# Optimization experiments

Measured on AMD Instinct MI355X. Metric: run time of the kernel, lower is better.

The kernel has to match this reference:

```python
import jax, jax.numpy as jnp
from jax import lax
import numpy as np

B, C, H, W = 16, 64, 256, 256
K = 4


def setup_inputs() -> dict:
    key = jax.random.key(0)
    k1, k2, k3, k4 = jax.random.split(key, 4)
    x = jax.random.normal(k1, (B, C, H, W), dtype=jnp.float32)
    weight = jax.random.normal(k2, (K, C, 3, 3), dtype=jnp.float32)
    # attn 1x1 conv: weight [K, C] (squeezed 1x1 spatial), bias [K]
    attn_w = jax.random.normal(k3, (K, C), dtype=jnp.float32) * (1.0 / np.sqrt(C))
    attn_b = jax.random.normal(k4, (K,), dtype=jnp.float32) * 0.01
    return {"x": x, "weight": weight, "attn_w": attn_w, "attn_b": attn_b}


def reference(x, weight, attn_w, attn_b):
    # 1x1 conv -> logits [B, K, H, W], then softmax over the K kernels
    logits = jnp.einsum("bchw,kc->bkhw", x, attn_w) + attn_b[None, :, None, None]
    attn = jax.nn.softmax(logits, axis=1)
    # One grouped call producing all K single-channel conv outputs: [B, K, H, W]
    conv = lax.conv_general_dilated(
        x, weight,
        window_strides=(1, 1), padding="SAME",
        dimension_numbers=("NCHW", "OIHW", "NCHW"),
    )
    # attention-weighted mixture, summed over kernels -> [B, 1, H, W]
    return jnp.sum(conv * attn, axis=1, keepdims=True)
```

## Files before the change

kernel.cpp:

```cpp
#include <hip/hip_runtime.h>


typedef _Float16 half2_t __attribute__((ext_vector_type(2)));
typedef unsigned int uint;

#define HH 256
#define WW 256
#define CH 64
#define PLANE (HH * WW)
#define NT 512
#define TR 32
#define TC 64
#define NG 32
#define ROWS 34
#define NC4 18
#define LDSS 73
#define BUF_DW (ROWS * LDSS)
#define TU (ROWS * NC4)
#define NS 2

#define WPK_N 1152
#define APK_OFF 1152

__device__ __forceinline__ uint pkrtz(float a, float b) {
    return __builtin_bit_cast(uint, __builtin_amdgcn_cvt_pkrtz(a, b));
}

__device__ __forceinline__ float dot2(uint a, uint b, float c) {
#if __has_builtin(__builtin_amdgcn_fdot2)
    return __builtin_amdgcn_fdot2(__builtin_bit_cast(half2_t, a),
                                  __builtin_bit_cast(half2_t, b), c, false);
#else
    half2_t ha = __builtin_bit_cast(half2_t, a);
    half2_t hb = __builtin_bit_cast(half2_t, b);
    return c + (float)ha[0] * (float)hb[0] + (float)ha[1] * (float)hb[1];
#endif
}

__global__ void kwdc_pack(const float* __restrict__ weight,
                          const float* __restrict__ attn_w,
                          uint* __restrict__ wsu) {
    int e = blockIdx.x * 256 + threadIdx.x;
    if (e < WPK_N) {
        int k = e / 288, rem = e % 288, pair = rem / 9, tap = rem % 9;
        int c0 = 2 * pair;
        wsu[e] = pkrtz(weight[(k * CH + c0) * 9 + tap],
                       weight[(k * CH + c0 + 1) * 9 + tap]);
    } else if (e < WPK_N + 128) {
        int e2 = e - WPK_N;
        int k = e2 / 32, pair = e2 % 32;
        int c0 = 2 * pair;
        wsu[APK_OFF + e2] = pkrtz(attn_w[k * CH + c0], attn_w[k * CH + c0 + 1]);
    }
}

__global__ __launch_bounds__(NT, 4) void kwdc_main(
    const float* __restrict__ x,
    const uint*  __restrict__ wsu,
    const float* __restrict__ attn_b,
    float* __restrict__ out)
{
    __shared__ uint lds[2][BUF_DW];

    const int tid = threadIdx.x;

    const int fid = blockIdx.x;
    const int tw = (fid >> 3) & 3;
    const int th = fid & 7;
    const int b  = fid >> 5;

    const int r  = tid >> 4;
    const int cg = tid & 15;
    const int wb = cg * 4;

    const int h0 = th * TR;
    const int w0 = tw * TC;

    const float* xb = x + (size_t)b * CH * PLANE;

    int  s_gofs[NS];
    int  s_lofs[NS];
    bool s_val[NS];
    bool s_act[NS];
#pragma unroll
    for (int s = 0; s < NS; ++s) {
        int i = tid + s * NT;
        bool act = i < TU;
        int col4 = i % NC4;
        int row  = i / NC4;
        int gh  = h0 + row - 1;
        int gw0 = w0 - 4 + col4 * 4;
        s_act[s]  = act;
        s_val[s]  = act && ((unsigned)gh < HH) && ((unsigned)gw0 < WW);
        s_gofs[s] = gh * WW + gw0;
        s_lofs[s] = row * LDSS + col4 * 4;
    }

    struct Unit { float4 a, b; };
    Unit stgA[NS], stgB[NS];

    auto load_set = [&](int g, Unit* stg) {
#pragma unroll
        for (int s = 0; s < NS; ++s) {
            float4 va = {0.f, 0.f, 0.f, 0.f}, vb = va;
            if (s_val[s]) {
                const float* pa = xb + (size_t)(2 * g) * PLANE + s_gofs[s];
                va = *reinterpret_cast<const float4*>(pa);
                vb = *reinterpret_cast<const float4*>(pa + PLANE);
            }
            stg[s].a = va; stg[s].b = vb;
        }
    };

    auto store_set = [&](const Unit* stg, int buf) {
#pragma unroll
        for (int s = 0; s < NS; ++s) {
            if (s_act[s]) {
                uint* q = &lds[buf][s_lofs[s]];
                q[0] = pkrtz(stg[s].a.x, stg[s].b.x);
                q[1] = pkrtz(stg[s].a.y, stg[s].b.y);
                q[2] = pkrtz(stg[s].a.z, stg[s].b.z);
                q[3] = pkrtz(stg[s].a.w, stg[s].b.w);
            }
        }
    };

    float conv[4][4];
    float logit[4][4];
#pragma unroll
    for (int k = 0; k < 4; ++k)
#pragma unroll
        for (int p = 0; p < 4; ++p) { conv[k][p] = 0.f; logit[k][p] = 0.f; }

    load_set(0, stgA);
    store_set(stgA, 0);
    load_set(1, stgA);
    load_set(2, stgB);
    __syncthreads();

    for (int g = 0; g < NG; ++g) {
        const uint* tp = &lds[g & 1][r * LDSS + wb + 3];
        uint rv[3][6];
#pragma unroll
        for (int i = 0; i < 3; ++i)
#pragma unroll
            for (int j = 0; j < 6; ++j)
                rv[i][j] = tp[i * LDSS + j];

        uint w2[4][9];
        uint a2[4];
#pragma unroll
        for (int k = 0; k < 4; ++k) {
            const uint* wq = wsu + k * 288 + g * 9;
#pragma unroll
            for (int t = 0; t < 9; ++t) w2[k][t] = wq[t];
            a2[k] = wsu[APK_OFF + k * 32 + g];
        }

        if (g + 1 < NG) {
            Unit* setp = (g & 1) ? stgB : stgA;
            store_set(setp, (g + 1) & 1);
            if (g + 3 < NG) load_set(g + 3, setp);
        }

#pragma unroll
        for (int k = 0; k < 4; ++k) {
#pragma unroll
            for (int p = 0; p < 4; ++p) {
                float acc = conv[k][p];
                acc = dot2(rv[0][p],     w2[k][0], acc);
                acc = dot2(rv[0][p + 1], w2[k][1], acc);
                acc = dot2(rv[0][p + 2], w2[k][2], acc);
                acc = dot2(rv[1][p],     w2[k][3], acc);
                acc = dot2(rv[1][p + 1], w2[k][4], acc);
                acc = dot2(rv[1][p + 2], w2[k][5], acc);
                acc = dot2(rv[2][p],     w2[k][6], acc);
                acc = dot2(rv[2][p + 1], w2[k][7], acc);
                acc = dot2(rv[2][p + 2], w2[k][8], acc);
                conv[k][p] = acc;
                logit[k][p] = dot2(rv[1][p + 1], a2[k], logit[k][p]);
            }
        }
        __syncthreads();
    }

    const float b0 = attn_b[0], b1 = attn_b[1], b2 = attn_b[2], b3 = attn_b[3];
    float4 o;
    float* op = &o.x;
#pragma unroll
    for (int p = 0; p < 4; ++p) {
        float l0 = logit[0][p] + b0;
        float l1 = logit[1][p] + b1;
        float l2 = logit[2][p] + b2;
        float l3 = logit[3][p] + b3;
        float m = fmaxf(fmaxf(l0, l1), fmaxf(l2, l3));
        float e0 = __expf(l0 - m), e1 = __expf(l1 - m);
        float e2 = __expf(l2 - m), e3 = __expf(l3 - m);
        float s = e0 + e1 + e2 + e3;
        float num = conv[0][p] * e0 + conv[1][p] * e1
                  + conv[2][p] * e2 + conv[3][p] * e3;
        op[p] = num / s;
    }
    size_t oidx = (size_t)b * PLANE + (size_t)(h0 + r) * WW + (w0 + wb);
    *reinterpret_cast<float4*>(out + oidx) = o;
}

extern "C" void kernel_launch(void* const* d_in, const int* in_sizes, int n_in,
                              void* d_out, int out_size, void* d_ws, size_t ws_size,
                              hipStream_t stream) {
    const float* x      = (const float*)d_in[0];
    const float* weight = (const float*)d_in[1];
    const float* attn_w = (const float*)d_in[2];
    const float* attn_b = (const float*)d_in[3];
    float* out = (float*)d_out;
    uint*  wsu = (uint*)d_ws;

    kwdc_pack<<<dim3(5), 256, 0, stream>>>(weight, attn_w, wsu);
    kwdc_main<<<dim3(512), NT, 0, stream>>>(x, wsu, attn_b, out);
}
```

Baseline: 84.57 us.

## Retile to full-width 8-row strips to drop column halo loads

```diff
diff --git a/kernel.cpp b/kernel.cpp
--- a/kernel.cpp
+++ b/kernel.cpp
@@ -9,13 +9,12 @@
 #define CH 64
 #define PLANE (HH * WW)
 #define NT 512
-#define TR 32
-#define TC 64
+#define SR 8
+#define ROWS 10
 #define NG 32
-#define ROWS 34
-#define NC4 18
-#define LDSS 73
-#define BUF_DW (ROWS * LDSS)
+#define NC4 64
+#define P 259
+#define BUF_DW (ROWS * P)
 #define TU (ROWS * NC4)
 #define NS 2
 
@@ -65,16 +64,14 @@
     const int tid = threadIdx.x;
 
     const int fid = blockIdx.x;
-    const int tw = (fid >> 3) & 3;
-    const int th = fid & 7;
-    const int b  = fid >> 5;
-
-    const int r  = tid >> 4;
-    const int cg = tid & 15;
+    const int b   = fid & 15;
+    const int s   = fid >> 4;
+
+    const int h0 = s * SR;
+
+    const int tr = tid >> 6;
+    const int cg = tid & 63;
     const int wb = cg * 4;
-
-    const int h0 = th * TR;
-    const int w0 = tw * TC;
 
     const float* xb = x + (size_t)b * CH * PLANE;
 
@@ -83,17 +80,16 @@
     bool s_val[NS];
     bool s_act[NS];
 #pragma unroll
-    for (int s = 0; s < NS; ++s) {
-        int i = tid + s * NT;
+    for (int q = 0; q < NS; ++q) {
+        int i = tid + q * NT;
         bool act = i < TU;
-        int col4 = i % NC4;
-        int row  = i / NC4;
+        int col4 = i & 63;
+        int row  = i >> 6;
         int gh  = h0 + row - 1;
-        int gw0 = w0 - 4 + col4 * 4;
-        s_act[s]  = act;
-        s_val[s]  = act && ((unsigned)gh < HH) && ((unsigned)gw0 < WW);
-        s_gofs[s] = gh * WW + gw0;
-        s_lofs[s] = row * LDSS + col4 * 4;
+        s_act[q]  = act;
+        s_val[q]  = act && ((unsigned)gh < HH);
+        s_gofs[q] = gh * WW + col4 * 4;
+        s_lofs[q] = row * P + col4 * 4 + 1;
     }
 
     struct Unit { float4 a, b; };
@@ -101,26 +97,26 @@
 
     auto load_set = [&](int g, Unit* stg) {
 #pragma unroll
-        for (int s = 0; s < NS; ++s) {
+        for (int q = 0; q < NS; ++q) {
             float4 va = {0.f, 0.f, 0.f, 0.f}, vb = va;
-            if (s_val[s]) {
-                const float* pa = xb + (size_t)(2 * g) * PLANE + s_gofs[s];
+            if (s_val[q]) {
+                const float* pa = xb + (size_t)(2 * g) * PLANE + s_gofs[q];
                 va = *reinterpret_cast<const float4*>(pa);
                 vb = *reinterpret_cast<const float4*>(pa + PLANE);
             }
-            stg[s].a = va; stg[s].b = vb;
+            stg[q].a = va; stg[q].b = vb;
         }
     };
 
     auto store_set = [&](const Unit* stg, int buf) {
 #pragma unroll
-        for (int s = 0; s < NS; ++s) {
-            if (s_act[s]) {
-                uint* q = &lds[buf][s_lofs[s]];
-                q[0] = pkrtz(stg[s].a.x, stg[s].b.x);
-                q[1] = pkrtz(stg[s].a.y, stg[s].b.y);
-                q[2] = pkrtz(stg[s].a.z, stg[s].b.z);
-                q[3] = pkrtz(stg[s].a.w, stg[s].b.w);
+        for (int q = 0; q < NS; ++q) {
+            if (s_act[q]) {
+                uint* w = &lds[buf][s_lofs[q]];
+                w[0] = pkrtz(stg[q].a.x, stg[q].b.x);
+                w[1] = pkrtz(stg[q].a.y, stg[q].b.y);
+                w[2] = pkrtz(stg[q].a.z, stg[q].b.z);
+                w[3] = pkrtz(stg[q].a.w, stg[q].b.w);
             }
         }
     };
@@ -139,28 +135,30 @@
     __syncthreads();
 
     for (int g = 0; g < NG; ++g) {
-        const uint* tp = &lds[g & 1][r * LDSS + wb + 3];
+        const uint* tp = &lds[g & 1][tr * P + wb];
         uint rv[3][6];
 #pragma unroll
         for (int i = 0; i < 3; ++i)
 #pragma unroll
             for (int j = 0; j < 6; ++j)
-                rv[i][j] = tp[i * LDSS + j];
-
-        uint w2[4][9];
-        uint a2[4];
-#pragma unroll
-        for (int k = 0; k < 4; ++k) {
-            const uint* wq = wsu + k * 288 + g * 9;
-#pragma unroll
-            for (int t = 0; t < 9; ++t) w2[k][t] = wq[t];
-            a2[k] = wsu[APK_OFF + k * 32 + g];
-        }
+                rv[i][j] = tp[i * P + j];
+        if (cg == 0)  { rv[0][0] = 0; rv[1][0] = 0; rv[2][0] = 0; }
+        if (cg == 63) { rv[0][5] = 0; rv[1][5] = 0; rv[2][5] = 0; }
 
         if (g + 1 < NG) {
             Unit* setp = (g & 1) ? stgB : stgA;
             store_set(setp, (g + 1) & 1);
             if (g + 3 < NG) load_set(g + 3, setp);
+        }
+
+        uint w2[4][9];
+        uint a2[4];
+#pragma unroll
+        for (int k = 0; k < 4; ++k) {
+            const uint* wq = wsu + k * 288 + g * 9;
+#pragma unroll
+            for (int t = 0; t < 9; ++t) w2[k][t] = wq[t];
+            a2[k] = wsu[APK_OFF + k * 32 + g];
         }
 
 #pragma unroll
@@ -196,12 +194,12 @@
         float m = fmaxf(fmaxf(l0, l1), fmaxf(l2, l3));
         float e0 = __expf(l0 - m), e1 = __expf(l1 - m);
         float e2 = __expf(l2 - m), e3 = __expf(l3 - m);
-        float s = e0 + e1 + e2 + e3;
+        float sden = e0 + e1 + e2 + e3;
         float num = conv[0][p] * e0 + conv[1][p] * e1
                   + conv[2][p] * e2 + conv[3][p] * e3;
-        op[p] = num / s;
-    }
-    size_t oidx = (size_t)b * PLANE + (size_t)(h0 + r) * WW + (w0 + wb);
+        op[p] = num / sden;
+    }
+    size_t oidx = (size_t)b * PLANE + (size_t)(h0 + tr) * WW + wb;
     *reinterpret_cast<float4*>(out + oidx) = o;
 }
 
```

New measurement: 93.63 us. 10.7% more time.
